# Performance work log

Hardware: AMD Instinct MI355X
Metric: run time of the kernel (lower is better)

The kernel has to match this reference:

```python
import jax, jax.numpy as jnp
import numpy as np

EPS = 1e-5  # BatchNorm eps; eval mode with running_mean=0, running_var=1

def _bn(x, g, b):
    return x * (g / jnp.sqrt(1.0 + EPS)) + b

def _lrelu(x):
    return jnp.where(x >= 0, x, 0.2 * x)

def setup_inputs() -> dict:
    key = jax.random.key(0)
    ks = jax.random.split(key, 30)
    def w(i, shape, s=0.05):
        return jax.random.normal(ks[i], shape, dtype=jnp.float32) * s
    inp = {"x": jax.random.normal(ks[0], (8, 10, 4096), dtype=jnp.float32), "k": 20}
    inp.update(
        w1=w(1, (64, 9)),    g1=1.0 + w(2, (64,), 0.1),  b1=w(3, (64,), 0.1),
        w2=w(4, (64, 64)),   g2=1.0 + w(5, (64,), 0.1),  b2=w(6, (64,), 0.1),
        w3=w(7, (128, 128)), g3=1.0 + w(8, (128,), 0.1), b3=w(9, (128,), 0.1),
        w4=w(10, (256, 128)), g4=1.0 + w(11, (256,), 0.1), b4=w(12, (256,), 0.1),
        w5=w(13, (1024, 256)), g5=1.0 + w(14, (1024,), 0.1), b5=w(15, (1024,), 0.1),
        l1w=w(16, (512, 1472)), l1b=w(17, (512,), 0.1),
        g6=1.0 + w(18, (512,), 0.1), b6=w(19, (512,), 0.1),
        l2w=w(20, (256, 512)), l2b=w(21, (256,), 0.1),
        g7=1.0 + w(22, (256,), 0.1), b7=w(23, (256,), 0.1),
        l3w=w(24, (2, 256)), l3b=w(25, (2,), 0.1),
    )
    return inp

def reference(x, k, w1, g1, b1, w2, g2, b2, w3, g3, b3, w4, g4, b4, w5, g5, b5,
              l1w, l1b, g6, b6, l2w, l2b, g7, b7, l3w, l3b):
    B, C, N = x.shape
    # --- kNN on xyz (first 3 channels); topk of negative squared distance ---
    xyz = x[:, :3, :]
    xx = jnp.sum(xyz * xyz, axis=1)                        # [B,N]
    inner = jnp.einsum('bcn,bcm->bnm', xyz, xyz)           # [B,N,N]
    pd = 2.0 * inner - xx[:, :, None] - xx[:, None, :]     # -||xi-xj||^2
    idx = jax.lax.top_k(pd, k)[1]                          # [B,N,k]
    # --- neighbor gather + edge features (xyz_i, rgb_i, rgb_i - rgb_j) ---
    xt = jnp.transpose(x, (0, 2, 1))                       # [B,N,C]
    nbr = xt[jnp.arange(B)[:, None, None], idx]            # [B,N,k,C]
    xyz_i = jnp.broadcast_to(xt[:, :, None, :3], (B, N, k, 3))
    rgb_i = jnp.broadcast_to(xt[:, :, None, 3:6], (B, N, k, 3))
    f = jnp.concatenate([xyz_i, rgb_i, rgb_i - nbr[..., 3:6]], axis=-1)  # [B,N,k,9]
    # --- EdgeConv MLPs (1x1 convs) + max over neighbors ---
    h = _lrelu(_bn(jnp.einsum('bnkc,oc->bnko', f, w1), g1, b1))
    h = _lrelu(_bn(jnp.einsum('bnkc,oc->bnko', h, w2), g2, b2))
    x1 = jnp.max(h, axis=2)                                # [B,N,64]
    x2 = _lrelu(_bn(jnp.einsum('bnc,oc->bno', jnp.concatenate([x1, x1], -1), w3), g3, b3))  # [B,N,128]
    x3 = _lrelu(_bn(jnp.einsum('bnc,oc->bno', x2, w4), g4, b4))  # [B,N,256]
    x4 = jnp.max(x3, axis=1)                               # [B,256] global max pool
    # conv5 applied to x4 repeated over N; max over identical copies == itself
    xg = _lrelu(_bn(x4 @ w5.T, g5, b5))                    # [B,1024]
    feat = jnp.concatenate([jnp.broadcast_to(xg[:, None, :], (B, N, 1024)), x3, x2, x1], axis=-1)  # [B,N,1472]
    h = _lrelu(_bn(feat @ l1w.T + l1b, g6, b6))            # dropout = identity (eval)
    h = _lrelu(_bn(h @ l2w.T + l2b, g7, b7))
    out = h @ l3w.T + l3b                                  # [B,N,num_classes]
    return jnp.transpose(out, (0, 2, 1))                   # [B,num_classes,N]
```

## Files before the change

kernel.cpp:

```cpp
#include <hip/hip_runtime.h>


#define KNN 20
#define NPID 32768
#define RS 0.99999500003750f

#define X3_PO 8388608
#define X2_PO 4194304
#define X1_PO 2097152

typedef unsigned short ushort_t;
typedef unsigned int u32;
typedef __attribute__((ext_vector_type(8))) short bf16x8;
typedef __attribute__((ext_vector_type(4))) float f32x4;

#define LDS_PTR(p) ((__attribute__((address_space(3))) void*)(p))
#define GLB_PTR(p) ((const __attribute__((address_space(1))) void*)(p))

__device__ __forceinline__ float lrelu(float z) { return z >= 0.f ? z : 0.2f * z; }
__device__ __forceinline__ unsigned short f2bf(float f) {
  unsigned int u = __float_as_uint(f);
  return (unsigned short)((u + 0x7fffu + ((u >> 16) & 1u)) >> 16);
}
__device__ __forceinline__ float bf2f(unsigned short h) { return __uint_as_float((unsigned int)h << 16); }
__device__ __forceinline__ u32 pack2(u32 e0, u32 e1) { return (e1 << 16) | (e0 & 0xffffu); }
__device__ __forceinline__ f32x4 mfma16(uint4 a, uint4 b, f32x4 c) {
  return __builtin_amdgcn_mfma_f32_16x16x32_bf16(
      __builtin_bit_cast(bf16x8, a), __builtin_bit_cast(bf16x8, b), c, 0, 0, 0);
}

__global__ __launch_bounds__(256) void xyzw_kernel(const float* __restrict__ x, float4* __restrict__ xyzw) {
  const int i = blockIdx.x * 256 + threadIdx.x;
  const int b = i >> 12, n = i & 4095;
  const float* xb = x + (size_t)b * 40960;
  const float px = xb[n], py = xb[4096 + n], pz = xb[8192 + n];
  const float xx = __fadd_rn(__fadd_rn(__fmul_rn(px, px), __fmul_rn(py, py)), __fmul_rn(pz, pz));
  float4 v; v.x = px; v.y = py; v.z = pz; v.w = xx;
  xyzw[i] = v;
}

__global__ __launch_bounds__(1024) void knn_kernel(const float4* __restrict__ xyzw, int* __restrict__ idxo) {
  __shared__ __align__(16) float4 pt[4096];
  __shared__ float cval[16][64];
  __shared__ int cidx[16][64];
  const int tid = threadIdx.x, lane = tid & 63, wave = tid >> 6;
  const int pid = blockIdx.x * 16 + wave;
  const int b = pid >> 12, n = pid & 4095;
  const float4* xw = xyzw + ((size_t)b << 12);
#pragma unroll
  for (int r = 0; r < 4; ++r) {
    const int chunk = wave * 4 + r;
    __builtin_amdgcn_global_load_lds(GLB_PTR(xw + chunk * 64 + lane),
                                     LDS_PTR((char*)pt + chunk * 1024), 16, 0, 0);
  }
  const float4 P = xw[n];
  const float px = P.x, py = P.y, pz = P.z, xxn = P.w;
  __syncthreads();
  float d[64];
  float lmax = -3.4e38f;
#pragma unroll
  for (int j = 0; j < 64; ++j) {
    const float4 Q = pt[j * 64 + lane];
    const float inner = __fadd_rn(__fadd_rn(__fmul_rn(px, Q.x), __fmul_rn(py, Q.y)), __fmul_rn(pz, Q.z));
    const float pd = __fsub_rn(__fsub_rn(__fmul_rn(2.0f, inner), xxn), Q.w);
    d[j] = pd;
    lmax = fmaxf(lmax, pd);
  }
  float v = lmax;
#pragma unroll
  for (int k = 2; k <= 64; k <<= 1) {
#pragma unroll
    for (int j = k >> 1; j > 0; j >>= 1) {
      const float ov = __shfl_xor(v, j, 64);
      const bool keepMax = (((lane & k) == 0) == ((lane & j) == 0));
      v = keepMax ? fmaxf(v, ov) : fminf(v, ov);
    }
  }
  const float t0 = __shfl(v, 19, 64);
  int base = 0;
#pragma unroll
  for (int j = 0; j < 64; ++j) {
    const bool take = (d[j] >= t0);
    const unsigned long long mk = __ballot(take);
    if (take) {
      const int pos = base + __popcll(mk & ((1ull << lane) - 1ull));
      if (pos < 64) {
        cval[wave][pos] = d[j];
        cidx[wave][pos] = (j << 6) + lane;
      }
    }
    base += (int)__popcll(mk);
  }
  const int C = base;
  int* out = idxo + (size_t)pid * KNN;
  if (C <= 64) {
    unsigned long long key = 0ull;
    if (lane < C) {
      const unsigned int u = __float_as_uint(cval[wave][lane]);
      const unsigned int ou = (u & 0x80000000u) ? ~u : (u | 0x80000000u);
      key = ((unsigned long long)ou << 32) | (unsigned long long)(0xFFFFFFFFu - (unsigned int)cidx[wave][lane]);
    }
#pragma unroll
    for (int k = 2; k <= 64; k <<= 1) {
#pragma unroll
      for (int j = k >> 1; j > 0; j >>= 1) {
        const unsigned long long ok = (unsigned long long)__shfl_xor((long long)key, j, 64);
        const bool keepMax = (((lane & k) == 0) == ((lane & j) == 0));
        const bool gt = key > ok;
        key = (keepMax == gt) ? key : ok;
      }
    }
    if (lane < KNN) out[lane] = (int)(0xFFFFFFFFu - (unsigned int)key);
  } else {
    unsigned long long used = 0ull;
#pragma unroll 1
    for (int it = 0; it < KNN; ++it) {
      float lv = -3.4e38f;
      int li = 1 << 30;
#pragma unroll
      for (int j = 0; j < 64; ++j) {
        if (!((used >> j) & 1ull) && d[j] > lv) {
          lv = d[j];
          li = (j << 6) + lane;
        }
      }
      float bv = lv;
      int bi = li;
#pragma unroll
      for (int s = 1; s < 64; s <<= 1) {
        const float ovv = __shfl_xor(bv, s, 64);
        const int oii = __shfl_xor(bi, s, 64);
        if (ovv > bv || (ovv == bv && oii < bi)) { bv = ovv; bi = oii; }
      }
      if (lane == 0) out[it] = bi;
      if ((bi & 63) == lane) used |= 1ull << (bi >> 6);
    }
  }
}

__global__ __launch_bounds__(256) void edge_kernel(const float* __restrict__ x, const int* __restrict__ idxi,
    const float* __restrict__ w1, const float* __restrict__ g1, const float* __restrict__ b1,
    const ushort_t* __restrict__ w2p, const float* __restrict__ g2, const float* __restrict__ b2,
    ushort_t* __restrict__ x1o) {
  __shared__ u32 hstage[4][16][64];
  const int tid = threadIdx.x, lane = tid & 63, wave = tid >> 6;
  const int fr = lane & 15, kg = lane >> 4;
  const int pbase = blockIdx.x * 64 + wave * 16;
  const int b = (blockIdx.x * 64) >> 12;
  const float* xq = x + (size_t)b * 40960;

  const int nA = (pbase + fr) & 4095;
  float cv[6]; ushort_t chv[6], clv[6];
#pragma unroll
  for (int j = 0; j < 6; ++j) {
    cv[j] = xq[j * 4096 + nA];
    chv[j] = f2bf(cv[j]);
    clv[j] = f2bf(cv[j] - bf2f(chv[j]));
  }
  const float crv = cv[3], cgv = cv[4], cbv = cv[5];

  u32 aC0 = 0, aC1 = 0, aC2 = 0, aC3 = 0;
  if (kg == 0) { aC0 = pack2(chv[0], chv[1]); aC1 = pack2(chv[2], chv[3]); aC2 = pack2(chv[4], chv[5]); }
  else if (kg == 1) { aC0 = (u32)chv[0] << 16; aC1 = pack2(chv[1], chv[2]); aC2 = pack2(chv[3], chv[4]); aC3 = chv[5]; }
  else if (kg == 2) { aC1 = pack2(clv[0], clv[1]); aC2 = pack2(clv[2], clv[3]); aC3 = pack2(clv[4], clv[5]); }

  float s1v[4], t1v[4], s2v[4], t2v[4];
#pragma unroll
  for (int fj = 0; fj < 4; ++fj) {
    const int och = fj * 16 + fr;
    s1v[fj] = g1[och] * RS; t1v[fj] = b1[och];
    s2v[fj] = g2[och] * RS; t2v[fj] = b2[och];
  }

  uint4 w1Bv[4];
#pragma unroll
  for (int fj = 0; fj < 4; ++fj) {
    const int och = fj * 16 + fr;
    ushort_t wh[9], wl[9];
#pragma unroll
    for (int j = 0; j < 9; ++j) {
      const float wv = w1[och * 9 + j];
      wh[j] = f2bf(wv);
      wl[j] = f2bf(wv - bf2f(wh[j]));
    }
    uint4 q;
    if (kg == 0)      { q.x = pack2(wh[0], wh[1]); q.y = pack2(wh[2], wh[3]); q.z = pack2(wh[4], wh[5]); q.w = pack2(wh[6], wh[7]); }
    else if (kg == 1) { q.x = pack2(wh[8], wl[0]); q.y = pack2(wl[1], wl[2]); q.z = pack2(wl[3], wl[4]); q.w = pack2(wl[5], wl[6]); }
    else if (kg == 2) { q.x = pack2(wl[7], wl[8]); q.y = pack2(wh[0], wh[1]); q.z = pack2(wh[2], wh[3]); q.w = pack2(wh[4], wh[5]); }
    else              { q.x = pack2(wh[6], wh[7]); q.y = pack2(wh[8], 0);     q.z = 0;                   q.w = 0; }
    w1Bv[fj] = q;
  }

  uint4 w2Bh[4][2], w2Bl[4][2];
#pragma unroll
  for (int fj = 0; fj < 4; ++fj) {
    const int och = fj * 16 + fr;
#pragma unroll
    for (int sub = 0; sub < 2; ++sub) {
      const ushort_t* ph = w2p + och * 64 + sub * 32 + kg * 8;
      w2Bh[fj][sub] = *(const uint4*)ph;
      w2Bl[fj][sub] = *(const uint4*)(ph + 4096);
    }
  }

  const int prow = (pbase + fr) * KNN;
  int miA = idxi[prow];
  int miN = idxi[prow + 1];
  float pr = xq[12288 + miA], pg = xq[16384 + miA], pb = xq[20480 + miA];

  f32x4 xm[4];
#pragma unroll
  for (int fj = 0; fj < 4; ++fj) { xm[fj][0] = -3.4e38f; xm[fj][1] = -3.4e38f; xm[fj][2] = -3.4e38f; xm[fj][3] = -3.4e38f; }
  const f32x4 zz = {0.f, 0.f, 0.f, 0.f};

#pragma unroll 1
  for (int kk = 0; kk < KNN; ++kk) {
    const float nrv = pr, ngv = pg, nbv = pb;
    if (kk < KNN - 1) { pr = xq[12288 + miN]; pg = xq[16384 + miN]; pb = xq[20480 + miN]; }
    if (kk < KNN - 2) { miN = idxi[prow + kk + 2]; }

    const float dr = crv - nrv, dg = cgv - ngv, db = cbv - nbv;
    const ushort_t drh = f2bf(dr), dgh = f2bf(dg), dbh = f2bf(db);
    const ushort_t drl = f2bf(dr - bf2f(drh)), dgl = f2bf(dg - bf2f(dgh)), dbl = f2bf(db - bf2f(dbh));

    uint4 aF;
    if (kg == 0)      { aF.x = aC0; aF.y = aC1; aF.z = aC2; aF.w = pack2(drh, dgh); }
    else if (kg == 1) { aF.x = aC0 | dbh; aF.y = aC1; aF.z = aC2; aF.w = aC3 | ((u32)drh << 16); }
    else if (kg == 2) { aF.x = pack2(dgh, dbh); aF.y = aC1; aF.z = aC2; aF.w = aC3; }
    else              { aF.x = pack2(drl, dgl); aF.y = (u32)dbl; aF.z = 0; aF.w = 0; }

    f32x4 h1a[4];
#pragma unroll
    for (int fj = 0; fj < 4; ++fj) h1a[fj] = mfma16(aF, w1Bv[fj], zz);

#pragma unroll
    for (int fj = 0; fj < 4; ++fj)
#pragma unroll
      for (int r = 0; r < 4; ++r) {
        float z = h1a[fj][r] * s1v[fj] + t1v[fj];
        z = fmaxf(z, 0.2f * z);
        const ushort_t hi = f2bf(z), lo = f2bf(z - bf2f(hi));
        const int pC = kg * 4 + r;
        hstage[wave][pC][(fj * 16 + fr) ^ ((pC & 7) << 3)] = ((u32)hi << 16) | lo;
      }

    f32x4 a2[4] = {zz, zz, zz, zz};
#pragma unroll
    for (int sub = 0; sub < 2; ++sub) {
      const u32* rp = &hstage[wave][fr][(sub * 32 + kg * 8) ^ ((fr & 7) << 3)];
      const uint4 q0 = *(const uint4*)rp;
      const uint4 q1 = *(const uint4*)(rp + 4);
      uint4 ah, al;
      ah.x = __builtin_amdgcn_perm(q0.y, q0.x, 0x07060302u); al.x = __builtin_amdgcn_perm(q0.y, q0.x, 0x05040100u);
      ah.y = __builtin_amdgcn_perm(q0.w, q0.z, 0x07060302u); al.y = __builtin_amdgcn_perm(q0.w, q0.z, 0x05040100u);
      ah.z = __builtin_amdgcn_perm(q1.y, q1.x, 0x07060302u); al.z = __builtin_amdgcn_perm(q1.y, q1.x, 0x05040100u);
      ah.w = __builtin_amdgcn_perm(q1.w, q1.z, 0x07060302u); al.w = __builtin_amdgcn_perm(q1.w, q1.z, 0x05040100u);
#pragma unroll
      for (int fj = 0; fj < 4; ++fj) {
        a2[fj] = mfma16(ah, w2Bh[fj][sub], a2[fj]);
        a2[fj] = mfma16(ah, w2Bl[fj][sub], a2[fj]);
        a2[fj] = mfma16(al, w2Bh[fj][sub], a2[fj]);
      }
    }

#pragma unroll
    for (int fj = 0; fj < 4; ++fj)
#pragma unroll
      for (int r = 0; r < 4; ++r) {
        float z = a2[fj][r] * s2v[fj] + t2v[fj];
        z = fmaxf(z, 0.2f * z);
        xm[fj][r] = fmaxf(xm[fj][r], z);
      }
  }

#pragma unroll
  for (int fj = 0; fj < 4; ++fj)
#pragma unroll
    for (int r = 0; r < 4; ++r) {
      const size_t e = (size_t)(pbase + kg * 4 + r) * 64 + fj * 16 + fr;
      const float v = xm[fj][r];
      const ushort_t hi = f2bf(v);
      x1o[e] = hi;
      x1o[X1_PO + e] = f2bf(v - bf2f(hi));
    }
}

__global__ __launch_bounds__(256) void prep_kernel(const float* __restrict__ w3, const float* __restrict__ w4,
    const float* __restrict__ l1w, const float* __restrict__ l2w, const float* __restrict__ w2,
    ushort_t* __restrict__ w3fp, ushort_t* __restrict__ w4p,
    ushort_t* __restrict__ l1wp, ushort_t* __restrict__ l2wp, ushort_t* __restrict__ w2p) {
  const int i = blockIdx.x * 256 + threadIdx.x;
  float f; ushort_t* hp; int n, j;
  if (i < 8192) {
    const int o = i >> 6, c = i & 63;
    f = w3[o * 128 + c] + w3[o * 128 + 64 + c];
    hp = w3fp; n = 8192; j = i;
  } else if (i < 8192 + 32768) {
    j = i - 8192; f = w4[j]; hp = w4p; n = 32768;
  } else if (i < 8192 + 32768 + 131072) {
    j = i - 8192 - 32768; f = l2w[j]; hp = l2wp; n = 131072;
  } else if (i < 172032 + 229376) {
    j = i - 172032;
    const int row = j / 448, col = j - row * 448;
    f = l1w[row * 1472 + 1024 + col];
    hp = l1wp; n = 229376;
  } else if (i < 401408 + 4096) {
    j = i - 401408; f = w2[j]; hp = w2p; n = 4096;
  } else return;
  const unsigned short h = f2bf(f);
  hp[j] = h;
  hp[n + j] = f2bf(f - bf2f(h));
}

template <int MODE, int OUTF32>
__global__ __launch_bounds__(256) void gemm_bf16(
    const ushort_t* __restrict__ A, const ushort_t* __restrict__ W, void* __restrict__ outv,
    const int Ktot, const int Nout, const int n_tiles,
    const int aPO, const int wPO, const int outPO,
    const float* __restrict__ gg, const float* __restrict__ bb,
    const float* __restrict__ linb, const int do_lrelu,
    const float* __restrict__ ybp, const ushort_t* __restrict__ x3,
    const ushort_t* __restrict__ x2, const ushort_t* __restrict__ x1) {
  __shared__ __align__(16) ushort_t lds[32768];
  const int tid = threadIdx.x, lane = tid & 63, wid = tid >> 6;
  const int nwg = gridDim.x;
  int id = (blockIdx.x & 7) * (nwg >> 3) + (blockIdx.x >> 3);
  const int mt = id / n_tiles, nt = id - mt * n_tiles;
  const int m0 = mt * 128, o0 = nt * 128;
  const int fr = lane & 15, kg = lane >> 4;
  const int wr = wid >> 1, wc = wid & 1;
  const int srow = lane >> 3, sslot = lane & 7;
  int rA[4], rB[4];
#pragma unroll
  for (int i = 0; i < 4; ++i) { rA[i] = wr * 64 + i * 16 + fr; rB[i] = wc * 64 + i * 16 + fr; }
  f32x4 acc[4][4] = {};
  const ushort_t* srcB = (wid == 2) ? W : W + wPO;
  const ushort_t* srcA0 = (MODE == 0) ? ((wid == 0) ? A : A + aPO) : nullptr;
  const int pl = (wid == 1);

  for (int kc = 0; kc < Ktot; kc += 64) {
#pragma unroll
    for (int c = 0; c < 16; ++c) {
      const int row = c * 8 + srow;
      const int rslot = sslot ^ (row & 7);
      const int k = kc + rslot * 8;
      const ushort_t* q;
      if (wid >= 2) {
        q = srcB + (size_t)(o0 + row) * Ktot + k;
      } else if (MODE == 0) {
        q = srcA0 + (size_t)(m0 + row) * Ktot + k;
      } else {
        const int m = m0 + row;
        if (k < 256)      q = x3 + pl * X3_PO + (size_t)m * 256 + k;
        else if (k < 384) q = x2 + pl * X2_PO + (size_t)m * 128 + (k - 256);
        else              q = x1 + pl * X1_PO + (size_t)m * 64 + (k - 384);
      }
      __builtin_amdgcn_global_load_lds(GLB_PTR(q), LDS_PTR(&lds[wid * 8192 + c * 512]), 16, 0, 0);
    }
    __syncthreads();
#pragma unroll
    for (int k0 = 0; k0 < 64; k0 += 32) {
      const int ks = (k0 >> 3) + kg;
      bf16x8 ah[4], al[4], bh[4], bl[4];
#pragma unroll
      for (int i = 0; i < 4; ++i) {
        const int off = rA[i] * 64 + ((ks ^ (rA[i] & 7)) << 3);
        ah[i] = *(const bf16x8*)&lds[off];
        al[i] = *(const bf16x8*)&lds[8192 + off];
      }
#pragma unroll
      for (int j = 0; j < 4; ++j) {
        const int off = rB[j] * 64 + ((ks ^ (rB[j] & 7)) << 3);
        bh[j] = *(const bf16x8*)&lds[16384 + off];
        bl[j] = *(const bf16x8*)&lds[24576 + off];
      }
#pragma unroll
      for (int i = 0; i < 4; ++i)
#pragma unroll
        for (int j = 0; j < 4; ++j) {
          acc[i][j] = __builtin_amdgcn_mfma_f32_16x16x32_bf16(ah[i], bh[j], acc[i][j], 0, 0, 0);
          acc[i][j] = __builtin_amdgcn_mfma_f32_16x16x32_bf16(ah[i], bl[j], acc[i][j], 0, 0, 0);
          acc[i][j] = __builtin_amdgcn_mfma_f32_16x16x32_bf16(al[i], bh[j], acc[i][j], 0, 0, 0);
        }
    }
    __syncthreads();
  }
  float s[4], t[4];
#pragma unroll
  for (int j = 0; j < 4; ++j) {
    const int o = o0 + wc * 64 + j * 16 + fr;
    s[j] = gg[o] * RS;
    float add = linb ? linb[o] : 0.f;
    if (MODE == 1) add += ybp[((m0 >> 12) << 9) + o];
    t[j] = bb[o] + add * s[j];
  }
#pragma unroll
  for (int i = 0; i < 4; ++i) {
#pragma unroll
    for (int j = 0; j < 4; ++j) {
      const int col = o0 + wc * 64 + j * 16 + fr;
#pragma unroll
      for (int r = 0; r < 4; ++r) {
        const int row = m0 + wr * 64 + i * 16 + kg * 4 + r;
        float z = acc[i][j][r] * s[j] + t[j];
        if (do_lrelu) z = lrelu(z);
        if (OUTF32) {
          ((float*)outv)[(size_t)row * Nout + col] = z;
        } else {
          ushort_t* oh = (ushort_t*)outv;
          const unsigned short h = f2bf(z);
          oh[(size_t)row * Nout + col] = h;
          oh[outPO + (size_t)row * Nout + col] = f2bf(z - bf2f(h));
        }
      }
    }
  }
}

__global__ __launch_bounds__(256) void max_kernel(const ushort_t* __restrict__ x3, float* __restrict__ x4p) {
  __shared__ float red[4][64];
  const int bid = blockIdx.x;
  const int q = bid & 3, seg = (bid >> 2) & 7, b = bid >> 5;
  const int cl = threadIdx.x & 63, nl = threadIdx.x >> 6;
  const int c = (q << 6) + cl;
  float acc = -3.4e38f;
  const int n0 = seg * 512;
  for (int n = n0 + nl; n < n0 + 512; n += 4) {
    const size_t e = ((size_t)b * 4096 + n) * 256 + c;
    acc = fmaxf(acc, bf2f(x3[e]) + bf2f(x3[X3_PO + e]));
  }
  red[nl][cl] = acc;
  __syncthreads();
  if (threadIdx.x < 64) {
    x4p[((size_t)b * 8 + seg) * 256 + c] = fmaxf(fmaxf(red[0][cl], red[1][cl]), fmaxf(red[2][cl], red[3][cl]));
  }
}

__global__ __launch_bounds__(256) void x4_kernel(const float* __restrict__ x4p, float* __restrict__ x4f) {
  const int b = blockIdx.x, c = threadIdx.x;
  float v = x4p[(size_t)b * 2048 + c];
#pragma unroll
  for (int s = 1; s < 8; ++s) v = fmaxf(v, x4p[(size_t)b * 2048 + s * 256 + c]);
  x4f[b * 256 + c] = v;
}

__global__ __launch_bounds__(256) void xg_kernel(const float* __restrict__ x4f, const float* __restrict__ w5,
    const float* __restrict__ g5, const float* __restrict__ b5, float* __restrict__ xgf) {
  const int lane = threadIdx.x & 63, wave = threadIdx.x >> 6;
  const int o = blockIdx.x * 4 + wave;
  const int b = o >> 10, oc = o & 1023;
  const float4 xv = *(const float4*)&x4f[b * 256 + lane * 4];
  const float4 w = *(const float4*)&w5[(size_t)oc * 256 + lane * 4];
  float acc = xv.x * w.x + xv.y * w.y + xv.z * w.z + xv.w * w.w;
#pragma unroll
  for (int s = 1; s < 64; s <<= 1) acc += __shfl_xor(acc, s, 64);
  if (lane == 0) xgf[o] = lrelu(acc * (g5[oc] * RS) + b5[oc]);
}

__global__ __launch_bounds__(256) void yb_kernel(const float* __restrict__ xgf, const float* __restrict__ l1w,
    float* __restrict__ yb) {
  const int lane = threadIdx.x & 63, wave = threadIdx.x >> 6;
  const int o = blockIdx.x * 4 + wave;
  const int b = o >> 9, oc = o & 511;
  float acc = 0.f;
#pragma unroll
  for (int i = 0; i < 4; ++i) {
    const int k = i * 256 + lane * 4;
    const float4 w = *(const float4*)&l1w[(size_t)oc * 1472 + k];
    const float4 g = *(const float4*)&xgf[b * 1024 + k];
    acc += w.x * g.x + w.y * g.y + w.z * g.z + w.w * g.w;
  }
#pragma unroll
  for (int s = 1; s < 64; s <<= 1) acc += __shfl_xor(acc, s, 64);
  if (lane == 0) yb[o] = acc;
}

__global__ __launch_bounds__(256) void l3_kernel(const float* __restrict__ h6, const float* __restrict__ l3w,
    const float* __restrict__ l3b, float* __restrict__ out) {
  __shared__ float wl[512];
  const int tid = threadIdx.x;
  wl[tid] = l3w[tid]; wl[256 + tid] = l3w[256 + tid];
  __syncthreads();
  const int m = blockIdx.x * 256 + tid;
  float a0 = 0.f, a1 = 0.f;
#pragma unroll
  for (int c = 0; c < 256; c += 4) {
    const float4 h = *(const float4*)(h6 + (size_t)m * 256 + c);
    a0 += h.x * wl[c] + h.y * wl[c + 1] + h.z * wl[c + 2] + h.w * wl[c + 3];
    a1 += h.x * wl[256 + c] + h.y * wl[256 + c + 1] + h.z * wl[256 + c + 2] + h.w * wl[256 + c + 3];
  }
  const int b = m >> 12, n = m & 4095;
  out[(size_t)b * 8192 + n] = a0 + l3b[0];
  out[(size_t)b * 8192 + 4096 + n] = a1 + l3b[1];
}

extern "C" void kernel_launch(void* const* d_in, const int* in_sizes, int n_in,
                              void* d_out, int out_size, void* d_ws, size_t ws_size,
                              hipStream_t stream) {
  const float* x   = (const float*)d_in[0];
  const float* w1  = (const float*)d_in[2];
  const float* g1  = (const float*)d_in[3];
  const float* b1  = (const float*)d_in[4];
  const float* w2  = (const float*)d_in[5];
  const float* g2  = (const float*)d_in[6];
  const float* b2  = (const float*)d_in[7];
  const float* w3  = (const float*)d_in[8];
  const float* g3  = (const float*)d_in[9];
  const float* b3  = (const float*)d_in[10];
  const float* w4  = (const float*)d_in[11];
  const float* g4  = (const float*)d_in[12];
  const float* b4  = (const float*)d_in[13];
  const float* w5  = (const float*)d_in[14];
  const float* g5  = (const float*)d_in[15];
  const float* b5  = (const float*)d_in[16];
  const float* l1w = (const float*)d_in[17];
  const float* l1b = (const float*)d_in[18];
  const float* g6  = (const float*)d_in[19];
  const float* b6  = (const float*)d_in[20];
  const float* l2w = (const float*)d_in[21];
  const float* l2b = (const float*)d_in[22];
  const float* g7  = (const float*)d_in[23];
  const float* b7  = (const float*)d_in[24];
  const float* l3w = (const float*)d_in[25];
  const float* l3b = (const float*)d_in[26];
  float* outp = (float*)d_out;

  char* ws = (char*)d_ws;
  int*      idx  = (int*)(ws + 0);
  ushort_t* x1   = (ushort_t*)(ws + 2621440);
  ushort_t* x2   = (ushort_t*)(ws + 11010048);
  ushort_t* x3   = (ushort_t*)(ws + 27787264);
  ushort_t* w2p  = (ushort_t*)(ws + 61341696);
  float*    x4p  = (float*)(ws + 61341696);
  float*    xgf  = (float*)(ws + 61407232);
  float*    x4f  = (float*)(ws + 61440000);
  float*    ybp  = (float*)(ws + 61448192);
  ushort_t* w3fp = (ushort_t*)(ws + 61440000);
  ushort_t* w4p  = (ushort_t*)(ws + 61472768);
  ushort_t* l2wp = (ushort_t*)(ws + 61603840);
  ushort_t* l1wp = (ushort_t*)(ws + 62128128);
  ushort_t* h5   = (ushort_t*)(ws + 65142784);
  float4*   xyzw = (float4*)(ws + 132251648);
  float*    h6   = (float*)(ws + 11010048);

  xyzw_kernel<<<128, 256, 0, stream>>>(x, xyzw);
  knn_kernel<<<NPID / 16, 1024, 0, stream>>>(xyzw, idx);
  prep_kernel<<<1584, 256, 0, stream>>>(w3, w4, l1w, l2w, w2, w3fp, w4p, l1wp, l2wp, w2p);
  edge_kernel<<<NPID / 64, 256, 0, stream>>>(x, idx, w1, g1, b1, w2p, g2, b2, x1);
  gemm_bf16<0, 0><<<256, 256, 0, stream>>>(x1, w3fp, x2, 64, 128, 1, X1_PO, 8192, X2_PO,
                                           g3, b3, nullptr, 1, nullptr, nullptr, nullptr, nullptr);
  gemm_bf16<0, 0><<<512, 256, 0, stream>>>(x2, w4p, x3, 128, 256, 2, X2_PO, 32768, X3_PO,
                                           g4, b4, nullptr, 1, nullptr, nullptr, nullptr, nullptr);
  max_kernel<<<256, 256, 0, stream>>>(x3, x4p);
  x4_kernel<<<8, 256, 0, stream>>>(x4p, x4f);
  xg_kernel<<<2048, 256, 0, stream>>>(x4f, w5, g5, b5, xgf);
  yb_kernel<<<1024, 256, 0, stream>>>(xgf, l1w, ybp);
  gemm_bf16<1, 0><<<1024, 256, 0, stream>>>(nullptr, l1wp, h5, 448, 512, 4, 0, 229376, 16777216,
                                            g6, b6, l1b, 1, ybp, x3, x2, x1);
  gemm_bf16<0, 1><<<512, 256, 0, stream>>>(h5, l2wp, h6, 512, 256, 2, 16777216, 131072, 0,
                                           g7, b7, l2b, 1, nullptr, nullptr, nullptr, nullptr);
  l3_kernel<<<128, 256, 0, stream>>>(h6, l3w, l3b, outp);
}
```

Measured before the change: 273.5 us.

## Fuse global max-pool into conv4 GEMM epilogue and halve GEMM K-chunk

The conv4 GEMM epilogue now computes per-column maxima, reduces them in LDS with atomics on order-preserving encoded floats, and does a global atomicMax into a buffer that prep_kernel zeroes. This removes the separate max_kernel and x4_kernel and the re-read of x3. Separately, all GEMMs now stage K in 32-wide chunks with a new swizzle, halving LDS to 32KB. That may raise occupancy but doubles the barrier count per K.

```diff
diff --git a/kernel.cpp b/kernel.cpp
--- a/kernel.cpp
+++ b/kernel.cpp
@@ -24,6 +24,13 @@
 }
 __device__ __forceinline__ float bf2f(unsigned short h) { return __uint_as_float((unsigned int)h << 16); }
 __device__ __forceinline__ u32 pack2(u32 e0, u32 e1) { return (e1 << 16) | (e0 & 0xffffu); }
+__device__ __forceinline__ u32 encf(float f) {
+  const u32 u = __float_as_uint(f);
+  return (u >> 31) ? ~u : (u | 0x80000000u);
+}
+__device__ __forceinline__ float decf(u32 e) {
+  return __uint_as_float((e >> 31) ? (e ^ 0x80000000u) : ~e);
+}
 __device__ __forceinline__ f32x4 mfma16(uint4 a, uint4 b, f32x4 c) {
   return __builtin_amdgcn_mfma_f32_16x16x32_bf16(
       __builtin_bit_cast(bf16x8, a), __builtin_bit_cast(bf16x8, b), c, 0, 0, 0);
@@ -288,7 +295,8 @@
 __global__ __launch_bounds__(256) void prep_kernel(const float* __restrict__ w3, const float* __restrict__ w4,
     const float* __restrict__ l1w, const float* __restrict__ l2w, const float* __restrict__ w2,
     ushort_t* __restrict__ w3fp, ushort_t* __restrict__ w4p,
-    ushort_t* __restrict__ l1wp, ushort_t* __restrict__ l2wp, ushort_t* __restrict__ w2p) {
+    ushort_t* __restrict__ l1wp, ushort_t* __restrict__ l2wp, ushort_t* __restrict__ w2p,
+    u32* __restrict__ x4u) {
   const int i = blockIdx.x * 256 + threadIdx.x;
   float f; ushort_t* hp; int n, j;
   if (i < 8192) {
@@ -306,13 +314,16 @@
     hp = l1wp; n = 229376;
   } else if (i < 401408 + 4096) {
     j = i - 401408; f = w2[j]; hp = w2p; n = 4096;
+  } else if (i < 405504 + 2048) {
+    x4u[i - 405504] = 0u;
+    return;
   } else return;
   const unsigned short h = f2bf(f);
   hp[j] = h;
   hp[n + j] = f2bf(f - bf2f(h));
 }
 
-template <int MODE, int OUTF32>
+template <int MODE, int OUTF32, int DOMAX>
 __global__ __launch_bounds__(256) void gemm_bf16(
     const ushort_t* __restrict__ A, const ushort_t* __restrict__ W, void* __restrict__ outv,
     const int Ktot, const int Nout, const int n_tiles,
@@ -320,8 +331,9 @@
     const float* __restrict__ gg, const float* __restrict__ bb,
     const float* __restrict__ linb, const int do_lrelu,
     const float* __restrict__ ybp, const ushort_t* __restrict__ x3,
-    const ushort_t* __restrict__ x2, const ushort_t* __restrict__ x1) {
-  __shared__ __align__(16) ushort_t lds[32768];
+    const ushort_t* __restrict__ x2, const ushort_t* __restrict__ x1,
+    u32* __restrict__ x4u) {
+  __shared__ __align__(16) ushort_t lds[16384];
   const int tid = threadIdx.x, lane = tid & 63, wid = tid >> 6;
   const int nwg = gridDim.x;
   int id = (blockIdx.x & 7) * (nwg >> 3) + (blockIdx.x >> 3);
@@ -329,7 +341,6 @@
   const int m0 = mt * 128, o0 = nt * 128;
   const int fr = lane & 15, kg = lane >> 4;
   const int wr = wid >> 1, wc = wid & 1;
-  const int srow = lane >> 3, sslot = lane & 7;
   int rA[4], rB[4];
 #pragma unroll
   for (int i = 0; i < 4; ++i) { rA[i] = wr * 64 + i * 16 + fr; rB[i] = wc * 64 + i * 16 + fr; }
@@ -338,11 +349,11 @@
   const ushort_t* srcA0 = (MODE == 0) ? ((wid == 0) ? A : A + aPO) : nullptr;
   const int pl = (wid == 1);
 
-  for (int kc = 0; kc < Ktot; kc += 64) {
-#pragma unroll
-    for (int c = 0; c < 16; ++c) {
-      const int row = c * 8 + srow;
-      const int rslot = sslot ^ (row & 7);
+  for (int kc = 0; kc < Ktot; kc += 32) {
+#pragma unroll
+    for (int c = 0; c < 8; ++c) {
+      const int row = c * 16 + (lane >> 2);
+      const int rslot = (lane & 3) ^ ((row >> 1) & 3);
       const int k = kc + rslot * 8;
       const ushort_t* q;
       if (wid >= 2) {
@@ -355,34 +366,30 @@
         else if (k < 384) q = x2 + pl * X2_PO + (size_t)m * 128 + (k - 256);
         else              q = x1 + pl * X1_PO + (size_t)m * 64 + (k - 384);
       }
-      __builtin_amdgcn_global_load_lds(GLB_PTR(q), LDS_PTR(&lds[wid * 8192 + c * 512]), 16, 0, 0);
+      __builtin_amdgcn_global_load_lds(GLB_PTR(q), LDS_PTR(&lds[wid * 4096 + c * 512]), 16, 0, 0);
     }
     __syncthreads();
-#pragma unroll
-    for (int k0 = 0; k0 < 64; k0 += 32) {
-      const int ks = (k0 >> 3) + kg;
-      bf16x8 ah[4], al[4], bh[4], bl[4];
-#pragma unroll
-      for (int i = 0; i < 4; ++i) {
-        const int off = rA[i] * 64 + ((ks ^ (rA[i] & 7)) << 3);
-        ah[i] = *(const bf16x8*)&lds[off];
-        al[i] = *(const bf16x8*)&lds[8192 + off];
-      }
+    bf16x8 ah[4], al[4], bh[4], bl[4];
+#pragma unroll
+    for (int i = 0; i < 4; ++i) {
+      const int off = rA[i] * 32 + ((kg ^ ((rA[i] >> 1) & 3)) << 3);
+      ah[i] = *(const bf16x8*)&lds[off];
+      al[i] = *(const bf16x8*)&lds[4096 + off];
+    }
+#pragma unroll
+    for (int j = 0; j < 4; ++j) {
+      const int off = rB[j] * 32 + ((kg ^ ((rB[j] >> 1) & 3)) << 3);
+      bh[j] = *(const bf16x8*)&lds[8192 + off];
+      bl[j] = *(const bf16x8*)&lds[12288 + off];
+    }
+#pragma unroll
+    for (int i = 0; i < 4; ++i)
 #pragma unroll
       for (int j = 0; j < 4; ++j) {
-        const int off = rB[j] * 64 + ((ks ^ (rB[j] & 7)) << 3);
-        bh[j] = *(const bf16x8*)&lds[16384 + off];
-        bl[j] = *(const bf16x8*)&lds[24576 + off];
-      }
-#pragma unroll
-      for (int i = 0; i < 4; ++i)
-#pragma unroll
-        for (int j = 0; j < 4; ++j) {
-          acc[i][j] = __builtin_amdgcn_mfma_f32_16x16x32_bf16(ah[i], bh[j], acc[i][j], 0, 0, 0);
-          acc[i][j] = __builtin_amdgcn_mfma_f32_16x16x32_bf16(ah[i], bl[j], acc[i][j], 0, 0, 0);
-          acc[i][j] = __builtin_amdgcn_mfma_f32_16x16x32_bf16(al[i], bh[j], acc[i][j], 0, 0, 0);
-        }
-    }
+        acc[i][j] = __builtin_amdgcn_mfma_f32_16x16x32_bf16(ah[i], bh[j], acc[i][j], 0, 0, 0);
+        acc[i][j] = __builtin_amdgcn_mfma_f32_16x16x32_bf16(ah[i], bl[j], acc[i][j], 0, 0, 0);
+        acc[i][j] = __builtin_amdgcn_mfma_f32_16x16x32_bf16(al[i], bh[j], acc[i][j], 0, 0, 0);
+      }
     __syncthreads();
   }
   float s[4], t[4];
@@ -394,6 +401,7 @@
     if (MODE == 1) add += ybp[((m0 >> 12) << 9) + o];
     t[j] = bb[o] + add * s[j];
   }
+  float cm[4] = {-3.4e38f, -3.4e38f, -3.4e38f, -3.4e38f};
 #pragma unroll
   for (int i = 0; i < 4; ++i) {
 #pragma unroll
@@ -404,6 +412,7 @@
         const int row = m0 + wr * 64 + i * 16 + kg * 4 + r;
         float z = acc[i][j][r] * s[j] + t[j];
         if (do_lrelu) z = lrelu(z);
+        if (DOMAX) cm[j] = fmaxf(cm[j], z);
         if (OUTF32) {
           ((float*)outv)[(size_t)row * Nout + col] = z;
         } else {
@@ -415,43 +424,26 @@
       }
     }
   }
-}
-
-__global__ __launch_bounds__(256) void max_kernel(const ushort_t* __restrict__ x3, float* __restrict__ x4p) {
-  __shared__ float red[4][64];
-  const int bid = blockIdx.x;
-  const int q = bid & 3, seg = (bid >> 2) & 7, b = bid >> 5;
-  const int cl = threadIdx.x & 63, nl = threadIdx.x >> 6;
-  const int c = (q << 6) + cl;
-  float acc = -3.4e38f;
-  const int n0 = seg * 512;
-  for (int n = n0 + nl; n < n0 + 512; n += 4) {
-    const size_t e = ((size_t)b * 4096 + n) * 256 + c;
-    acc = fmaxf(acc, bf2f(x3[e]) + bf2f(x3[X3_PO + e]));
-  }
-  red[nl][cl] = acc;
-  __syncthreads();
-  if (threadIdx.x < 64) {
-    x4p[((size_t)b * 8 + seg) * 256 + c] = fmaxf(fmaxf(red[0][cl], red[1][cl]), fmaxf(red[2][cl], red[3][cl]));
-  }
-}
-
-__global__ __launch_bounds__(256) void x4_kernel(const float* __restrict__ x4p, float* __restrict__ x4f) {
-  const int b = blockIdx.x, c = threadIdx.x;
-  float v = x4p[(size_t)b * 2048 + c];
-#pragma unroll
-  for (int s = 1; s < 8; ++s) v = fmaxf(v, x4p[(size_t)b * 2048 + s * 256 + c]);
-  x4f[b * 256 + c] = v;
-}
-
-__global__ __launch_bounds__(256) void xg_kernel(const float* __restrict__ x4f, const float* __restrict__ w5,
+  if (DOMAX) {
+    __syncthreads();
+    u32* mcol = (u32*)lds;
+    if (tid < 128) mcol[tid] = 0u;
+    __syncthreads();
+#pragma unroll
+    for (int j = 0; j < 4; ++j) atomicMax(&mcol[wc * 64 + j * 16 + fr], encf(cm[j]));
+    __syncthreads();
+    if (tid < 128) atomicMax(&x4u[((m0 >> 12) << 8) + o0 + tid], mcol[tid]);
+  }
+}
+
+__global__ __launch_bounds__(256) void xg_kernel(const u32* __restrict__ x4u, const float* __restrict__ w5,
     const float* __restrict__ g5, const float* __restrict__ b5, float* __restrict__ xgf) {
   const int lane = threadIdx.x & 63, wave = threadIdx.x >> 6;
   const int o = blockIdx.x * 4 + wave;
   const int b = o >> 10, oc = o & 1023;
-  const float4 xv = *(const float4*)&x4f[b * 256 + lane * 4];
+  const uint4 xu = *(const uint4*)&x4u[b * 256 + lane * 4];
   const float4 w = *(const float4*)&w5[(size_t)oc * 256 + lane * 4];
-  float acc = xv.x * w.x + xv.y * w.y + xv.z * w.z + xv.w * w.w;
+  float acc = decf(xu.x) * w.x + decf(xu.y) * w.y + decf(xu.z) * w.z + decf(xu.w) * w.w;
 #pragma unroll
   for (int s = 1; s < 64; s <<= 1) acc += __shfl_xor(acc, s, 64);
   if (lane == 0) xgf[o] = lrelu(acc * (g5[oc] * RS) + b5[oc]);
@@ -531,9 +523,8 @@
   ushort_t* x2   = (ushort_t*)(ws + 11010048);
   ushort_t* x3   = (ushort_t*)(ws + 27787264);
   ushort_t* w2p  = (ushort_t*)(ws + 61341696);
-  float*    x4p  = (float*)(ws + 61341696);
+  u32*      x4u  = (u32*)(ws + 61358080);
   float*    xgf  = (float*)(ws + 61407232);
-  float*    x4f  = (float*)(ws + 61440000);
   float*    ybp  = (float*)(ws + 61448192);
   ushort_t* w3fp = (ushort_t*)(ws + 61440000);
   ushort_t* w4p  = (ushort_t*)(ws + 61472768);
@@ -545,19 +536,17 @@
 
   xyzw_kernel<<<128, 256, 0, stream>>>(x, xyzw);
   knn_kernel<<<NPID / 16, 1024, 0, stream>>>(xyzw, idx);
-  prep_kernel<<<1584, 256, 0, stream>>>(w3, w4, l1w, l2w, w2, w3fp, w4p, l1wp, l2wp, w2p);
+  prep_kernel<<<1592, 256, 0, stream>>>(w3, w4, l1w, l2w, w2, w3fp, w4p, l1wp, l2wp, w2p, x4u);
   edge_kernel<<<NPID / 64, 256, 0, stream>>>(x, idx, w1, g1, b1, w2p, g2, b2, x1);
-  gemm_bf16<0, 0><<<256, 256, 0, stream>>>(x1, w3fp, x2, 64, 128, 1, X1_PO, 8192, X2_PO,
-                                           g3, b3, nullptr, 1, nullptr, nullptr, nullptr, nullptr);
-  gemm_bf16<0, 0><<<512, 256, 0, stream>>>(x2, w4p, x3, 128, 256, 2, X2_PO, 32768, X3_PO,
-                                           g4, b4, nullptr, 1, nullptr, nullptr, nullptr, nullptr);
-  max_kernel<<<256, 256, 0, stream>>>(x3, x4p);
-  x4_kernel<<<8, 256, 0, stream>>>(x4p, x4f);
-  xg_kernel<<<2048, 256, 0, stream>>>(x4f, w5, g5, b5, xgf);
+  gemm_bf16<0, 0, 0><<<256, 256, 0, stream>>>(x1, w3fp, x2, 64, 128, 1, X1_PO, 8192, X2_PO,
+                                              g3, b3, nullptr, 1, nullptr, nullptr, nullptr, nullptr, nullptr);
+  gemm_bf16<0, 0, 1><<<512, 256, 0, stream>>>(x2, w4p, x3, 128, 256, 2, X2_PO, 32768, X3_PO,
+                                              g4, b4, nullptr, 1, nullptr, nullptr, nullptr, nullptr, x4u);
+  xg_kernel<<<2048, 256, 0, stream>>>(x4u, w5, g5, b5, xgf);
   yb_kernel<<<1024, 256, 0, stream>>>(xgf, l1w, ybp);
-  gemm_bf16<1, 0><<<1024, 256, 0, stream>>>(nullptr, l1wp, h5, 448, 512, 4, 0, 229376, 16777216,
-                                            g6, b6, l1b, 1, ybp, x3, x2, x1);
-  gemm_bf16<0, 1><<<512, 256, 0, stream>>>(h5, l2wp, h6, 512, 256, 2, 16777216, 131072, 0,
-                                           g7, b7, l2b, 1, nullptr, nullptr, nullptr, nullptr);
+  gemm_bf16<1, 0, 0><<<1024, 256, 0, stream>>>(nullptr, l1wp, h5, 448, 512, 4, 0, 229376, 16777216,
+                                               g6, b6, l1b, 1, ybp, x3, x2, x1, nullptr);
+  gemm_bf16<0, 1, 0><<<512, 256, 0, stream>>>(h5, l2wp, h6, 512, 256, 2, 16777216, 131072, 0,
+                                              g7, b7, l2b, 1, nullptr, nullptr, nullptr, nullptr, nullptr);
   l3_kernel<<<128, 256, 0, stream>>>(h6, l3w, l3b, outp);
 }
```

New measurement: 259.2 us. -5.2%, faster.
